# Kernel tuning notes

Hardware: AMD Instinct MI355X
Metric: run time of the kernel (lower is better)

The kernel has to match this reference:

```python
import jax, jax.numpy as jnp
import numpy as np

NUM_PIECE_TYPES = 7
NUM_COLORS = 3
NUM_CASTLING_STATES = 16
NUM_EP_STATES = 9
D = 256
B = 4096
EPS = 1e-5


def setup_inputs() -> dict:
    key = jax.random.key(0)
    ks = jax.random.split(key, 12)
    inp = {
        'piece_ids': jax.random.randint(ks[0], (B, 64), 0, NUM_PIECE_TYPES),
        'color_ids': jax.random.randint(ks[1], (B, 64), 0, NUM_COLORS),
        'turn': jax.random.randint(ks[2], (B,), 0, 2),
        'castling': jax.random.randint(ks[3], (B,), 0, NUM_CASTLING_STATES),
        'ep_file': jax.random.randint(ks[4], (B,), 0, NUM_EP_STATES),
        # learned parameters
        'piece_table': jax.random.normal(ks[5], (NUM_PIECE_TYPES, D), jnp.float32) * 0.02,
        'W': jax.random.normal(ks[6], (NUM_COLORS, D, D), jnp.float32) * (1.0 / np.sqrt(D)),
        'b': jax.random.normal(ks[7], (NUM_COLORS, D), jnp.float32) * 0.02,
        'square_table': jax.random.normal(ks[8], (64, D), jnp.float32) * 0.02,
        'turn_table': jax.random.normal(ks[9], (2, D), jnp.float32) * 0.02,
        'castling_table': jax.random.normal(ks[10], (NUM_CASTLING_STATES, D), jnp.float32) * 0.02,
        'ep_table': jax.random.normal(ks[11], (NUM_EP_STATES, D), jnp.float32) * 0.02,
        'gamma': jnp.ones((D,), jnp.float32),
        'beta': jnp.zeros((D,), jnp.float32),
    }
    return inp


def _layernorm(x, gamma, beta):
    mu = jnp.mean(x, axis=-1, keepdims=True)
    var = jnp.mean(jnp.square(x - mu), axis=-1, keepdims=True)
    return (x - mu) * jax.lax.rsqrt(var + EPS) * gamma + beta


def reference(piece_ids, color_ids, turn, castling, ep_file,
              piece_table, W, b, square_table, turn_table,
              castling_table, ep_table, gamma, beta):
    piece_emb = piece_table[piece_ids]                      # (B,64,D)
    # per-color linear: proj_stack[b,s,c] = piece_emb[b,s] @ W[c].T + b[c]
    proj_stack = jnp.einsum('bsd,cod->bsco', piece_emb, W) + b  # (B,64,C,D)
    # select the projection for each square's color (== one-hot mask + sum)
    idx = color_ids[..., None, None]                        # (B,64,1,1)
    sq_emb = jnp.take_along_axis(proj_stack, idx, axis=2)[:, :, 0, :]  # (B,64,D)
    sq_emb = sq_emb + square_table[None, :, :]              # add positional
    turn_tok = turn_table[turn][:, None, :]                 # (B,1,D)
    castle_tok = castling_table[castling][:, None, :]       # (B,1,D)
    ep_tok = ep_table[ep_file][:, None, :]                  # (B,1,D)
    tokens = jnp.concatenate([turn_tok, castle_tok, ep_tok, sq_emb], axis=1)  # (B,67,D)
    return _layernorm(tokens, gamma, beta)
```

## Files before the change

### kernel.cpp

```cpp
#include <hip/hip_runtime.h>


#define DIM 256
#define NPT 7
#define NCOL 3
#define NROWS_SQ (NPT * NCOL * 64)
#define ROW_TURN 1344
#define ROW_CASTLE 1346
#define ROW_EP 1362
#define NROWS_TOT 1371
#define EPSV 1e-5f

typedef float f32x4 __attribute__((ext_vector_type(4)));

__global__ void proj_kernel(const float* __restrict__ piece_table,
                            const float* __restrict__ W,
                            const float* __restrict__ bvec,
                            float* __restrict__ proj) {
    int e = blockIdx.x;
    int p = e / NCOL, c = e % NCOL;
    int d = threadIdx.x;
    __shared__ float pt[DIM];
    pt[d] = piece_table[p * DIM + d];
    __syncthreads();
    const float4* w4 = (const float4*)(W + (size_t)c * DIM * DIM + (size_t)d * DIM);
    float acc = bvec[c * DIM + d];
    #pragma unroll 8
    for (int k = 0; k < DIM / 4; ++k) {
        float4 w = w4[k];
        acc += w.x * pt[k * 4 + 0] + w.y * pt[k * 4 + 1]
             + w.z * pt[k * 4 + 2] + w.w * pt[k * 4 + 3];
    }
    proj[e * DIM + d] = acc;
}

__global__ void ln_table_kernel(const float* __restrict__ proj,
                                const float* __restrict__ square_table,
                                const float* __restrict__ turn_table,
                                const float* __restrict__ castling_table,
                                const float* __restrict__ ep_table,
                                const float* __restrict__ gamma,
                                const float* __restrict__ beta,
                                float* __restrict__ table) {
    int w = blockIdx.x * 4 + (threadIdx.x >> 6);
    int lane = threadIdx.x & 63;
    if (w >= NROWS_TOT) return;

    float4 x;
    if (w < NROWS_SQ) {
        int p = w / 192;
        int rem = w - p * 192;
        int c = rem >> 6;
        int s = rem & 63;
        float4 a = ((const float4*)(proj + (p * NCOL + c) * DIM))[lane];
        float4 q = ((const float4*)(square_table + s * DIM))[lane];
        x = make_float4(a.x + q.x, a.y + q.y, a.z + q.z, a.w + q.w);
    } else if (w < ROW_CASTLE) {
        x = ((const float4*)(turn_table + (w - ROW_TURN) * DIM))[lane];
    } else if (w < ROW_EP) {
        x = ((const float4*)(castling_table + (w - ROW_CASTLE) * DIM))[lane];
    } else {
        x = ((const float4*)(ep_table + (w - ROW_EP) * DIM))[lane];
    }

    float s = x.x + x.y + x.z + x.w;
    #pragma unroll
    for (int m = 1; m < 64; m <<= 1) s += __shfl_xor(s, m, 64);
    float mu = s * (1.0f / DIM);

    float dx = x.x - mu, dy = x.y - mu, dz = x.z - mu, dw = x.w - mu;
    float v = dx * dx + dy * dy + dz * dz + dw * dw;
    #pragma unroll
    for (int m = 1; m < 64; m <<= 1) v += __shfl_xor(v, m, 64);
    float inv = rsqrtf(v * (1.0f / DIM) + EPSV);

    float4 g = ((const float4*)gamma)[lane];
    float4 bb = ((const float4*)beta)[lane];
    float4 y = make_float4(dx * inv * g.x + bb.x,
                           dy * inv * g.y + bb.y,
                           dz * inv * g.z + bb.z,
                           dw * inv * g.w + bb.w);
    ((float4*)(table + (size_t)w * DIM))[lane] = y;
}

__global__ void gather_kernel(const int* __restrict__ piece_ids,
                              const int* __restrict__ color_ids,
                              const int* __restrict__ turn,
                              const int* __restrict__ castling,
                              const int* __restrict__ ep_file,
                              const float* __restrict__ table,
                              float* __restrict__ out,
                              int nrows) {
    int r = blockIdx.x * 4 + (threadIdx.x >> 6);
    if (r >= nrows) return;
    int lane = threadIdx.x & 63;
    int b = r / 67;
    int t = r - b * 67;
    int row;
    if (t == 0) {
        row = ROW_TURN + turn[b];
    } else if (t == 1) {
        row = ROW_CASTLE + castling[b];
    } else if (t == 2) {
        row = ROW_EP + ep_file[b];
    } else {
        int s = t - 3;
        int idx = b * 64 + s;
        row = piece_ids[idx] * (NCOL * 64) + color_ids[idx] * 64 + s;
    }
    f32x4 v = ((const f32x4*)(table + (size_t)row * DIM))[lane];
    __builtin_nontemporal_store(v, (f32x4*)(out + (size_t)r * DIM) + lane);
}

extern "C" void kernel_launch(void* const* d_in, const int* in_sizes, int n_in,
                              void* d_out, int out_size, void* d_ws, size_t ws_size,
                              hipStream_t stream) {
    const int*   piece_ids      = (const int*)d_in[0];
    const int*   color_ids      = (const int*)d_in[1];
    const int*   turn           = (const int*)d_in[2];
    const int*   castling       = (const int*)d_in[3];
    const int*   ep_file        = (const int*)d_in[4];
    const float* piece_table    = (const float*)d_in[5];
    const float* W              = (const float*)d_in[6];
    const float* bvec           = (const float*)d_in[7];
    const float* square_table   = (const float*)d_in[8];
    const float* turn_table     = (const float*)d_in[9];
    const float* castling_table = (const float*)d_in[10];
    const float* ep_table       = (const float*)d_in[11];
    const float* gamma          = (const float*)d_in[12];
    const float* beta           = (const float*)d_in[13];
    float* out = (float*)d_out;

    int B = in_sizes[0] / 64;
    int nrows = B * 67;

    float* proj  = (float*)d_ws;
    float* table = proj + NPT * NCOL * DIM;

    proj_kernel<<<NPT * NCOL, 256, 0, stream>>>(piece_table, W, bvec, proj);
    ln_table_kernel<<<(NROWS_TOT + 3) / 4, 256, 0, stream>>>(
        proj, square_table, turn_table, castling_table, ep_table, gamma, beta, table);
    gather_kernel<<<(nrows + 3) / 4, 256, 0, stream>>>(
        piece_ids, color_ids, turn, castling, ep_file, table, out, nrows);
}
```

Before: 61.96 us.

## Fuse layernorm into gather kernel, dropping precomputed normalized table

```diff
diff --git a/kernel.cpp b/kernel.cpp
--- a/kernel.cpp
+++ b/kernel.cpp
@@ -4,11 +4,6 @@
 #define DIM 256
 #define NPT 7
 #define NCOL 3
-#define NROWS_SQ (NPT * NCOL * 64)
-#define ROW_TURN 1344
-#define ROW_CASTLE 1346
-#define ROW_EP 1362
-#define NROWS_TOT 1371
 #define EPSV 1e-5f
 
 typedef float f32x4 __attribute__((ext_vector_type(4)));
@@ -34,82 +29,66 @@
     proj[e * DIM + d] = acc;
 }
 
-__global__ void ln_table_kernel(const float* __restrict__ proj,
-                                const float* __restrict__ square_table,
-                                const float* __restrict__ turn_table,
-                                const float* __restrict__ castling_table,
-                                const float* __restrict__ ep_table,
-                                const float* __restrict__ gamma,
-                                const float* __restrict__ beta,
-                                float* __restrict__ table) {
-    int w = blockIdx.x * 4 + (threadIdx.x >> 6);
-    int lane = threadIdx.x & 63;
-    if (w >= NROWS_TOT) return;
-
-    float4 x;
-    if (w < NROWS_SQ) {
-        int p = w / 192;
-        int rem = w - p * 192;
-        int c = rem >> 6;
-        int s = rem & 63;
-        float4 a = ((const float4*)(proj + (p * NCOL + c) * DIM))[lane];
-        float4 q = ((const float4*)(square_table + s * DIM))[lane];
-        x = make_float4(a.x + q.x, a.y + q.y, a.z + q.z, a.w + q.w);
-    } else if (w < ROW_CASTLE) {
-        x = ((const float4*)(turn_table + (w - ROW_TURN) * DIM))[lane];
-    } else if (w < ROW_EP) {
-        x = ((const float4*)(castling_table + (w - ROW_CASTLE) * DIM))[lane];
-    } else {
-        x = ((const float4*)(ep_table + (w - ROW_EP) * DIM))[lane];
-    }
-
-    float s = x.x + x.y + x.z + x.w;
-    #pragma unroll
-    for (int m = 1; m < 64; m <<= 1) s += __shfl_xor(s, m, 64);
-    float mu = s * (1.0f / DIM);
-
-    float dx = x.x - mu, dy = x.y - mu, dz = x.z - mu, dw = x.w - mu;
-    float v = dx * dx + dy * dy + dz * dz + dw * dw;
-    #pragma unroll
-    for (int m = 1; m < 64; m <<= 1) v += __shfl_xor(v, m, 64);
-    float inv = rsqrtf(v * (1.0f / DIM) + EPSV);
-
-    float4 g = ((const float4*)gamma)[lane];
-    float4 bb = ((const float4*)beta)[lane];
-    float4 y = make_float4(dx * inv * g.x + bb.x,
-                           dy * inv * g.y + bb.y,
-                           dz * inv * g.z + bb.z,
-                           dw * inv * g.w + bb.w);
-    ((float4*)(table + (size_t)w * DIM))[lane] = y;
-}
-
-__global__ void gather_kernel(const int* __restrict__ piece_ids,
-                              const int* __restrict__ color_ids,
-                              const int* __restrict__ turn,
-                              const int* __restrict__ castling,
-                              const int* __restrict__ ep_file,
-                              const float* __restrict__ table,
-                              float* __restrict__ out,
-                              int nrows) {
+__global__ void gather_ln_kernel(const int* __restrict__ piece_ids,
+                                 const int* __restrict__ color_ids,
+                                 const int* __restrict__ turn,
+                                 const int* __restrict__ castling,
+                                 const int* __restrict__ ep_file,
+                                 const float* __restrict__ proj,
+                                 const float* __restrict__ square_table,
+                                 const float* __restrict__ turn_table,
+                                 const float* __restrict__ castling_table,
+                                 const float* __restrict__ ep_table,
+                                 const float* __restrict__ gamma,
+                                 const float* __restrict__ beta,
+                                 float* __restrict__ out,
+                                 int nrows) {
     int r = blockIdx.x * 4 + (threadIdx.x >> 6);
     if (r >= nrows) return;
     int lane = threadIdx.x & 63;
     int b = r / 67;
     int t = r - b * 67;
-    int row;
-    if (t == 0) {
-        row = ROW_TURN + turn[b];
-    } else if (t == 1) {
-        row = ROW_CASTLE + castling[b];
-    } else if (t == 2) {
-        row = ROW_EP + ep_file[b];
-    } else {
+
+    const float* src;
+    const float* addp = nullptr;
+    if (t >= 3) {
         int s = t - 3;
         int idx = b * 64 + s;
-        row = piece_ids[idx] * (NCOL * 64) + color_ids[idx] * 64 + s;
+        src  = proj + (size_t)(piece_ids[idx] * NCOL + color_ids[idx]) * DIM;
+        addp = square_table + (size_t)s * DIM;
+    } else if (t == 0) {
+        src = turn_table + (size_t)turn[b] * DIM;
+    } else if (t == 1) {
+        src = castling_table + (size_t)castling[b] * DIM;
+    } else {
+        src = ep_table + (size_t)ep_file[b] * DIM;
     }
-    f32x4 v = ((const f32x4*)(table + (size_t)row * DIM))[lane];
-    __builtin_nontemporal_store(v, (f32x4*)(out + (size_t)r * DIM) + lane);
+
+    float4 x = ((const float4*)src)[lane];
+    if (addp) {
+        float4 q = ((const float4*)addp)[lane];
+        x.x += q.x; x.y += q.y; x.z += q.z; x.w += q.w;
+    }
+
+    float s1 = x.x + x.y + x.z + x.w;
+    float s2 = x.x * x.x + x.y * x.y + x.z * x.z + x.w * x.w;
+    #pragma unroll
+    for (int m = 1; m < 64; m <<= 1) {
+        s1 += __shfl_xor(s1, m, 64);
+        s2 += __shfl_xor(s2, m, 64);
+    }
+    float mu  = s1 * (1.0f / DIM);
+    float var = fmaxf(s2 * (1.0f / DIM) - mu * mu, 0.0f);
+    float inv = rsqrtf(var + EPSV);
+
+    float4 g  = ((const float4*)gamma)[lane];
+    float4 bb = ((const float4*)beta)[lane];
+    f32x4 y;
+    y.x = (x.x - mu) * inv * g.x + bb.x;
+    y.y = (x.y - mu) * inv * g.y + bb.y;
+    y.z = (x.z - mu) * inv * g.z + bb.z;
+    y.w = (x.w - mu) * inv * g.w + bb.w;
+    __builtin_nontemporal_store(y, (f32x4*)(out + (size_t)r * DIM) + lane);
 }
 
 extern "C" void kernel_launch(void* const* d_in, const int* in_sizes, int n_in,
@@ -133,13 +112,11 @@
 
     int B = in_sizes[0] / 64;
     int nrows = B * 67;
-
-    float* proj  = (float*)d_ws;
-    float* table = proj + NPT * NCOL * DIM;
+    float* proj = (float*)d_ws;
 
     proj_kernel<<<NPT * NCOL, 256, 0, stream>>>(piece_table, W, bvec, proj);
-    ln_table_kernel<<<(NROWS_TOT + 3) / 4, 256, 0, stream>>>(
-        proj, square_table, turn_table, castling_table, ep_table, gamma, beta, table);
-    gather_kernel<<<(nrows + 3) / 4, 256, 0, stream>>>(
-        piece_ids, color_ids, turn, castling, ep_file, table, out, nrows);
+    gather_ln_kernel<<<(nrows + 3) / 4, 256, 0, stream>>>(
+        piece_ids, color_ids, turn, castling, ep_file,
+        proj, square_table, turn_table, castling_table, ep_table,
+        gamma, beta, out, nrows);
 }
```

After: 71.26 us. 1.15x slower.
